# Kernel optimization log

Measured on AMD Instinct MI355X. Metric: run time of the kernel, lower is better.

The kernel has to match this reference:

```python
import jax, jax.numpy as jnp
import numpy as np

B, L, S, C, H = 2, 2048, 2048, 1024, 16
HD = C // H  # head_dim = 64


def setup_inputs() -> dict:
    key = jax.random.key(0)
    k0, k1, k2, k3, k4 = jax.random.split(key, 5)
    w_scale = 1.0 / np.sqrt(C).astype(np.float32)
    return {
        "x0": jax.random.normal(k0, (B, L, C), jnp.float32),
        "x1": jax.random.normal(k1, (B, S, C), jnp.float32),
        "Wqk": jax.random.normal(k2, (C, C), jnp.float32) * w_scale,
        "Wv": jax.random.normal(k3, (C, C), jnp.float32) * w_scale,
        "Wmerge": jax.random.normal(k4, (C, C), jnp.float32) * w_scale,
    }


def reference(x0, x1, Wqk, Wv, Wmerge):
    softmax_temp = HD ** -0.5
    scale = softmax_temp ** 0.5  # applied to both qk0 and qk1

    def split_heads(t):  # [B,N,C] -> [B,N,H,HD]
        return t.reshape(t.shape[0], t.shape[1], H, HD)

    # shared QK projection (same weight for both streams), torch Linear: y = x @ W^T
    qk0 = split_heads(x0 @ Wqk.T) * scale  # [B,L,H,HD]
    qk1 = split_heads(x1 @ Wqk.T) * scale  # [B,S,H,HD]
    v0 = split_heads(x0 @ Wv.T)            # [B,L,H,HD]
    v1 = split_heads(x1 @ Wv.T)            # [B,S,H,HD]

    # single similarity matrix reused for both softmax directions
    sim = jnp.einsum('blhd,bshd->bhls', qk0, qk1)  # [B,H,L,S]
    attn01 = jax.nn.softmax(sim, axis=-1)  # softmax over S (x0 attends x1)
    attn10 = jax.nn.softmax(sim, axis=-2)  # softmax over L (== softmax(sim^T, -1))

    o0 = jnp.einsum('bhls,bshd->blhd', attn01, v1).reshape(x0.shape[0], x0.shape[1], C)
    o1 = jnp.einsum('bhls,blhd->bshd', attn10, v0).reshape(x1.shape[0], x1.shape[1], C)

    return (o0 @ Wmerge.T, o1 @ Wmerge.T)
```

## Files before the change

### kernel.cpp

```cpp
#include <hip/hip_runtime.h>
#include <hip/hip_bf16.h>
#include <stdint.h>


typedef __attribute__((ext_vector_type(8))) short bf16x8;
typedef __attribute__((ext_vector_type(4))) float f32x4;
typedef __attribute__((ext_vector_type(16))) float f32x16;
typedef __attribute__((ext_vector_type(4))) unsigned int u32x4;
typedef __attribute__((ext_vector_type(2))) unsigned int u32x2;
typedef __bf16 bf16_2 __attribute__((ext_vector_type(2)));

typedef const __attribute__((address_space(1))) unsigned int gu32;
typedef __attribute__((address_space(3))) unsigned int lu32;

__device__ __forceinline__ unsigned short f2bf(float f) {
  unsigned int u = __builtin_bit_cast(unsigned int, f);
  u += 0x7fffu + ((u >> 16) & 1u);
  return (unsigned short)(u >> 16);
}

__device__ __forceinline__ unsigned int cvtpk(float lo, float hi_) {
  bf16_2 t = { (__bf16)lo, (__bf16)hi_ };
  return __builtin_bit_cast(unsigned int, t);
}

__device__ __forceinline__ unsigned short f2bf_hw(float f) {
  return __builtin_bit_cast(unsigned short, (__bf16)f);
}

__global__ void cvt_x(const float* __restrict__ x0, const float* __restrict__ x1,
                      unsigned short* __restrict__ dst) {
  const long NX = 4194304;
  int y = blockIdx.y;
  const float* src = y ? x1 : x0;
  long i = ((long)blockIdx.x * 256 + threadIdx.x) * 8;
  float4 a = *(const float4*)(src + i);
  float4 b = *(const float4*)(src + i + 4);
  union { unsigned short u[8]; bf16x8 v; } r;
  r.u[0] = f2bf(a.x); r.u[1] = f2bf(a.y); r.u[2] = f2bf(a.z); r.u[3] = f2bf(a.w);
  r.u[4] = f2bf(b.x); r.u[5] = f2bf(b.y); r.u[6] = f2bf(b.z); r.u[7] = f2bf(b.w);
  *(bf16x8*)(dst + y * NX + i) = r.v;
}

__global__ void cvt_w(const float* __restrict__ w0, const float* __restrict__ w1,
                      const float* __restrict__ w2, unsigned short* __restrict__ dst) {
  const long NW = 1048576;
  int y = blockIdx.y;
  const float* src = (y == 0) ? w0 : ((y == 1) ? w1 : w2);
  long i = ((long)blockIdx.x * 256 + threadIdx.x) * 8;
  float4 a = *(const float4*)(src + i);
  float4 b = *(const float4*)(src + i + 4);
  union { unsigned short u[8]; bf16x8 v; } r;
  r.u[0] = f2bf(a.x); r.u[1] = f2bf(a.y); r.u[2] = f2bf(a.z); r.u[3] = f2bf(a.w);
  r.u[4] = f2bf(b.x); r.u[5] = f2bf(b.y); r.u[6] = f2bf(b.z); r.u[7] = f2bf(b.w);
  *(bf16x8*)(dst + y * NW + i) = r.v;
}

template<int OUTF32>
__global__ __launch_bounds__(256, 2)
void gemm_bt(const unsigned short* __restrict__ A, const unsigned short* __restrict__ B,
             void* __restrict__ C, int M, int N, int K, float scale) {
  __shared__ unsigned short As[128 * 32];
  __shared__ unsigned short Bs[128 * 32];
  const int tid = threadIdx.x;
  const int lane = tid & 63, w = tid >> 6;
  const int il = lane & 15, g = lane >> 4;
  const int wr = w >> 1, wc = w & 1;
  const int bm = blockIdx.y * 128, bn = blockIdx.x * 128;
  f32x4 acc[4][4];
#pragma unroll
  for (int m = 0; m < 4; ++m)
#pragma unroll
    for (int n = 0; n < 4; ++n) acc[m][n] = (f32x4){0.f, 0.f, 0.f, 0.f};

  const int crow = lane >> 2, ccol = (lane & 3) * 8;
  const int ch0 = w * 2, ch1 = w * 2 + 1;
  const unsigned short* pa0 = A + (long)(bm + ch0 * 16 + crow) * K + ccol;
  const unsigned short* pa1 = A + (long)(bm + ch1 * 16 + crow) * K + ccol;
  const unsigned short* pb0 = B + (long)(bn + ch0 * 16 + crow) * K + ccol;
  const unsigned short* pb1 = B + (long)(bn + ch1 * 16 + crow) * K + ccol;

  for (int k0 = 0; k0 < K; k0 += 32) {
    __builtin_amdgcn_global_load_lds((gu32*)(pa0 + k0), (lu32*)(As + ch0 * 512), 16, 0, 0);
    __builtin_amdgcn_global_load_lds((gu32*)(pa1 + k0), (lu32*)(As + ch1 * 512), 16, 0, 0);
    __builtin_amdgcn_global_load_lds((gu32*)(pb0 + k0), (lu32*)(Bs + ch0 * 512), 16, 0, 0);
    __builtin_amdgcn_global_load_lds((gu32*)(pb1 + k0), (lu32*)(Bs + ch1 * 512), 16, 0, 0);
    __syncthreads();
    bf16x8 av[4], bv[4];
#pragma unroll
    for (int m = 0; m < 4; ++m)
      av[m] = *(const bf16x8*)(As + (wr * 64 + m * 16 + il) * 32 + g * 8);
#pragma unroll
    for (int n = 0; n < 4; ++n)
      bv[n] = *(const bf16x8*)(Bs + (wc * 64 + n * 16 + il) * 32 + g * 8);
#pragma unroll
    for (int m = 0; m < 4; ++m)
#pragma unroll
      for (int n = 0; n < 4; ++n)
        acc[m][n] = __builtin_amdgcn_mfma_f32_16x16x32_bf16(av[m], bv[n], acc[m][n], 0, 0, 0);
    __syncthreads();
  }

#pragma unroll
  for (int m = 0; m < 4; ++m) {
    long row0 = bm + wr * 64 + m * 16 + g * 4;
#pragma unroll
    for (int n = 0; n < 4; ++n) {
      long col = bn + wc * 64 + n * 16 + il;
#pragma unroll
      for (int r = 0; r < 4; ++r) {
        float v = acc[m][n][r] * scale;
        if (OUTF32) ((float*)C)[(row0 + r) * (long)N + col] = v;
        else        ((unsigned short*)C)[(row0 + r) * (long)N + col] = f2bf(v);
      }
    }
  }
}


#define QSTAGEA(BUF, MH, TT)                                                              \
  {                                                                                       \
    long kc = (long)(TT) * 64 + sslot * 8;                                                \
    const unsigned short* s0 = Ag + (long)(bm + (MH) * 64 + srow) * 1024 + kc;            \
    const unsigned short* s1 = Ag + (long)(bm + 128 + (MH) * 64 + srow) * 1024 + kc;      \
    __builtin_amdgcn_global_load_lds((gu32*)s0, (lu32*)(smem + ((BUF)*2+(MH))*8192 + dbase), 16, 0, 0);        \
    __builtin_amdgcn_global_load_lds((gu32*)s1, (lu32*)(smem + ((BUF)*2+(MH))*8192 + 4096 + dbase), 16, 0, 0); \
  }

#define QSTAGEB(BUF, NH, TT)                                                              \
  {                                                                                       \
    long kc = (long)(TT) * 64 + sslot * 8;                                                \
    const unsigned short* s0 = Bg + (long)(bnn + ((srow >> 5) * 64) + (NH) * 32 + (srow & 31)) * 1024 + kc;        \
    const unsigned short* s1 = Bg + (long)(bnn + (((64 + srow) >> 5) * 64) + (NH) * 32 + (srow & 31)) * 1024 + kc; \
    __builtin_amdgcn_global_load_lds((gu32*)s0, (lu32*)(smem + 32768 + ((BUF)*2+(NH))*8192 + dbase), 16, 0, 0);        \
    __builtin_amdgcn_global_load_lds((gu32*)s1, (lu32*)(smem + 32768 + ((BUF)*2+(NH))*8192 + 4096 + dbase), 16, 0, 0); \
  }

#define QCOMPUTE(RBUF, MH, NH)                                                            \
  {                                                                                       \
    const unsigned short* Ar = smem + ((RBUF)*2+(MH))*8192 + (wr * 64 + il) * 64;         \
    const unsigned short* Br = smem + 32768 + ((RBUF)*2+(NH))*8192 + (wc * 32 + il) * 64; \
    bf16x8 av[4][2], bv[2][2];                                                            \
    _Pragma("unroll")                                                                     \
    for (int mp = 0; mp < 4; ++mp)                                                        \
      _Pragma("unroll")                                                                   \
      for (int ks = 0; ks < 2; ++ks)                                                      \
        av[mp][ks] = *(const bf16x8*)(Ar + mp * 1024 + (((ks * 4 + g) ^ sw) * 8));        \
    _Pragma("unroll")                                                                     \
    for (int np = 0; np < 2; ++np)                                                        \
      _Pragma("unroll")                                                                   \
      for (int ks = 0; ks < 2; ++ks)                                                      \
        bv[np][ks] = *(const bf16x8*)(Br + np * 1024 + (((ks * 4 + g) ^ sw) * 8));        \
    _Pragma("unroll")                                                                     \
    for (int mp = 0; mp < 4; ++mp)                                                        \
      _Pragma("unroll")                                                                   \
      for (int np = 0; np < 2; ++np) {                                                    \
        acc[(MH)*4+mp][(NH)*2+np] = __builtin_amdgcn_mfma_f32_16x16x32_bf16(av[mp][0], bv[np][0], acc[(MH)*4+mp][(NH)*2+np], 0, 0, 0); \
        acc[(MH)*4+mp][(NH)*2+np] = __builtin_amdgcn_mfma_f32_16x16x32_bf16(av[mp][1], bv[np][1], acc[(MH)*4+mp][(NH)*2+np], 0, 0, 0); \
      }                                                                                   \
  }

#define QEND(W4)                                                                          \
  {                                                                                       \
    if (W4) asm volatile("s_waitcnt vmcnt(4)" ::: "memory");                              \
    asm volatile("" ::: "memory");                                                        \
    __builtin_amdgcn_s_barrier();                                                         \
    asm volatile("" ::: "memory");                                                        \
  }

__global__ __launch_bounds__(512, 2)
void gemm_qkv8(const unsigned short* __restrict__ Ag, const unsigned short* __restrict__ Bg,
               unsigned short* __restrict__ C0, unsigned short* __restrict__ vt, float scale0) {
  extern __shared__ unsigned short smem[];
  const int tid = threadIdx.x;
  const int lane = tid & 63, wid = tid >> 6;
  const int il = lane & 15, g = lane >> 4;
  const int wr = wid >> 2, wc = wid & 3;
  const int sw = il & 7;
  const int bm = blockIdx.y * 256, bnn = blockIdx.x * 256;

  const int srow = tid >> 3;
  const int sslot = (tid & 7) ^ ((tid >> 3) & 7);
  const int dbase = (tid >> 6) * 512;

  f32x4 acc[8][4];
#pragma unroll
  for (int m = 0; m < 8; ++m)
#pragma unroll
    for (int n = 0; n < 4; ++n) acc[m][n] = (f32x4){0.f, 0.f, 0.f, 0.f};

  QSTAGEA(0, 0, 0); QSTAGEA(0, 1, 0); QSTAGEB(0, 0, 0); QSTAGEB(0, 1, 0);
  QSTAGEB(1, 0, 1); QSTAGEA(1, 1, 1);
  __syncthreads();

#pragma unroll 1
  for (int i = 0; i < 8; ++i) {
    const int t1 = 2 * i + 1, t2 = (2 * i + 2) & 15, t3 = (2 * i + 3) & 15;
    QSTAGEA(1, 0, t1); QCOMPUTE(0, 0, 0); QEND(0);
    QSTAGEB(1, 1, t1); QCOMPUTE(0, 1, 0); QEND(0);
    QSTAGEB(0, 0, t2); QCOMPUTE(0, 1, 1); QEND(0);
    QSTAGEA(0, 1, t2); QCOMPUTE(0, 0, 1); QEND(1);
    QSTAGEA(0, 0, t2); QCOMPUTE(1, 0, 0); QEND(0);
    QSTAGEB(0, 1, t2); QCOMPUTE(1, 1, 0); QEND(0);
    QSTAGEB(1, 0, t3); QCOMPUTE(1, 1, 1); QEND(0);
    QSTAGEA(1, 1, t3); QCOMPUTE(1, 0, 1); QEND(1);
  }
  __syncthreads();

  if (bnn < 1024) {
#pragma unroll
    for (int m = 0; m < 8; ++m) {
      long row0 = bm + wr * 128 + m * 16 + g * 4;
#pragma unroll
      for (int n = 0; n < 4; ++n) {
        long col = bnn + wc * 64 + n * 16 + il;
#pragma unroll
        for (int r = 0; r < 4; ++r)
          C0[(row0 + r) * 1024 + col] = f2bf(acc[m][n][r] * scale0);
      }
    }
  } else {
    unsigned short (*T)[264] = (unsigned short (*)[264])smem;
    const int s = bm >> 11;
#pragma unroll 1
    for (int p = 0; p < 2; ++p) {
      if ((wc >> 1) == p) {
#pragma unroll
        for (int m = 0; m < 8; ++m) {
          int rl = wr * 128 + m * 16 + g * 4;
#pragma unroll
          for (int n = 0; n < 4; ++n) {
            int cl = (wc & 1) * 64 + n * 16 + il;
            u32x2 pk = { cvtpk(acc[m][n][0], acc[m][n][1]), cvtpk(acc[m][n][2], acc[m][n][3]) };
            *(u32x2*)&T[cl][rl] = pk;
          }
        }
      }
      __syncthreads();
      int cl2 = tid & 127, portion = tid >> 7;
      int col = (bnn - 1024) + p * 128 + cl2;
      unsigned short* dst = vt + (((long)(s * 16 + (col >> 6))) * 64 + (col & 63)) * 2048
                               + (bm & 2047) + portion * 64;
#pragma unroll
      for (int j = 0; j < 8; ++j)
        *(bf16x8*)(dst + j * 8) = *(const bf16x8*)&T[cl2][portion * 64 + j * 8];
      __syncthreads();
    }
  }
}

__global__ __launch_bounds__(256, 4)
void attn_kernel(const unsigned short* __restrict__ qk,
                 const unsigned short* __restrict__ vt,
                 unsigned short* __restrict__ o) {
  __shared__ unsigned short sK[2][4096];
  __shared__ unsigned short sV[2][4096];
  int bid = blockIdx.x;
  int lb = (bid & 7) * 128 + (bid >> 3);
  int tid = threadIdx.x;
  int w = tid >> 6, lane = tid & 63;
  int u = lb * 4 + w;
  int dir = u >> 11, bh = (u >> 6) & 31, qu = u & 63;
  int b = bh >> 4, h = bh & 15;
  int q = lane & 31, hi = lane >> 5;

  long qrow0 = (dir ? 4096L : 0L) + b * 2048L + (long)qu * 32L;
  long krow0 = (dir ? 0L : 4096L) + b * 2048L;
  int vs = dir ? b : 2 + b;
  long vrow0 = (long)(vs * 16 + h) * 64;

  const unsigned short* Qp = qk + (qrow0 + q) * 1024 + h * 64 + hi * 8;

  int srow = tid >> 3;
  int sc = ((tid & 7) * 8) ^ ((srow & 7) << 3);
  const unsigned short* kg = qk + (krow0 + srow) * 1024 + h * 64 + sc;
  const unsigned short* vg = vt + (vrow0 + srow) * 2048 + sc;
  const int wbase = w * 512;

#define STAGE(BUF, T)                                                                    \
  {                                                                                      \
    long jj = (long)(T) * 64;                                                            \
    __builtin_amdgcn_global_load_lds((gu32*)(kg + jj * 1024),        (lu32*)(sK[BUF] + wbase),        16, 0, 0); \
    __builtin_amdgcn_global_load_lds((gu32*)(kg + (jj + 32) * 1024), (lu32*)(sK[BUF] + wbase + 2048), 16, 0, 0); \
    __builtin_amdgcn_global_load_lds((gu32*)(vg + jj),               (lu32*)(sV[BUF] + wbase),        16, 0, 0); \
    __builtin_amdgcn_global_load_lds((gu32*)(vg + jj + 32 * 2048),   (lu32*)(sV[BUF] + wbase + 2048), 16, 0, 0); \
  }

  bf16x8 qf[4];
#pragma unroll
  for (int ds = 0; ds < 4; ++ds)
    qf[ds] = *(const bf16x8*)(Qp + ds * 16);

  f32x16 z16;
#pragma unroll
  for (int j = 0; j < 16; ++j) z16[j] = 0.f;
  f32x16 accO[2];
  accO[0] = z16; accO[1] = z16;
  f32x16 lsum = z16;
  const short oneb = (short)0x3F80;
  const bf16x8 ones = {oneb, oneb, oneb, oneb, oneb, oneb, oneb, oneb};

  STAGE(0, 0);
  __syncthreads();

#pragma unroll 1
  for (int t = 0; t < 32; ++t) {
    int cur = t & 1;
    if (t < 31) STAGE(cur ^ 1, t + 1);

    bf16x8 kf[8], vf[8];
    int cswz = (q & 7) << 3;
#pragma unroll
    for (int kb = 0; kb < 2; ++kb)
#pragma unroll
      for (int ds = 0; ds < 4; ++ds)
        kf[kb * 4 + ds] = *(const bf16x8*)(&sK[cur][(kb * 32 + q) * 64 + ((ds * 16 + hi * 8) ^ cswz)]);
#pragma unroll
    for (int ks = 0; ks < 4; ++ks)
#pragma unroll
      for (int dn = 0; dn < 2; ++dn)
        vf[ks * 2 + dn] = *(const bf16x8*)(&sV[cur][(dn * 32 + q) * 64 + ((ks * 16 + hi * 8) ^ cswz)]);

    f32x16 st0 = __builtin_amdgcn_mfma_f32_32x32x16_bf16(kf[0], qf[0], z16, 0, 0, 0);
    f32x16 st1 = __builtin_amdgcn_mfma_f32_32x32x16_bf16(kf[4], qf[0], z16, 0, 0, 0);
#pragma unroll
    for (int ds = 1; ds < 4; ++ds)
      st0 = __builtin_amdgcn_mfma_f32_32x32x16_bf16(kf[ds], qf[ds], st0, 0, 0, 0);
#pragma unroll
    for (int ds = 1; ds < 4; ++ds)
      st1 = __builtin_amdgcn_mfma_f32_32x32x16_bf16(kf[4 + ds], qf[ds], st1, 0, 0, 0);

#pragma unroll
    for (int j = 0; j < 16; ++j) {
      st0[j] = __builtin_amdgcn_exp2f(st0[j]);
      st1[j] = __builtin_amdgcn_exp2f(st1[j]);
    }

    bf16x8 pa[4];
#pragma unroll
    for (int ks = 0; ks < 4; ++ks) {
      int m0 = (ks & 1) * 8;
      unsigned int a0, a1, b0, b1;
      if (ks < 2) {
        a0 = cvtpk(st0[m0],     st0[m0 + 1]); a1 = cvtpk(st0[m0 + 2], st0[m0 + 3]);
        b0 = cvtpk(st0[m0 + 4], st0[m0 + 5]); b1 = cvtpk(st0[m0 + 6], st0[m0 + 7]);
      } else {
        a0 = cvtpk(st1[m0],     st1[m0 + 1]); a1 = cvtpk(st1[m0 + 2], st1[m0 + 3]);
        b0 = cvtpk(st1[m0 + 4], st1[m0 + 5]); b1 = cvtpk(st1[m0 + 6], st1[m0 + 7]);
      }
      u32x2 r0 = __builtin_amdgcn_permlane32_swap(a0, b0, false, false);
      u32x2 r1 = __builtin_amdgcn_permlane32_swap(a1, b1, false, false);
      u32x4 uu = {r0[0], r1[0], r0[1], r1[1]};
      pa[ks] = __builtin_bit_cast(bf16x8, uu);
    }
#pragma unroll
    for (int ks = 0; ks < 4; ++ks)
      lsum = __builtin_amdgcn_mfma_f32_32x32x16_bf16(pa[ks], ones, lsum, 0, 0, 0);
#pragma unroll
    for (int ks = 0; ks < 4; ++ks)
#pragma unroll
      for (int dn = 0; dn < 2; ++dn)
        accO[dn] = __builtin_amdgcn_mfma_f32_32x32x16_bf16(pa[ks], vf[ks * 2 + dn], accO[dn], 0, 0, 0);

    __syncthreads();
  }
#undef STAGE

#pragma unroll
  for (int r = 0; r < 16; ++r) {
    int row = (r & 3) + 8 * (r >> 2) + 4 * hi;
    float invr = 1.f / lsum[r];
    long orow = qrow0 + row;
#pragma unroll
    for (int dn = 0; dn < 2; ++dn)
      o[orow * 1024 + h * 64 + dn * 32 + q] = f2bf_hw(accO[dn][r] * invr);
  }
}

extern "C" void kernel_launch(void* const* d_in, const int* in_sizes, int n_in,
                              void* d_out, int out_size, void* d_ws, size_t ws_size,
                              hipStream_t stream) {
  const float* x0 = (const float*)d_in[0];
  const float* x1 = (const float*)d_in[1];
  const float* Wqk = (const float*)d_in[2];
  const float* Wv = (const float*)d_in[3];
  const float* Wm = (const float*)d_in[4];
  float* out = (float*)d_out;

  const long NX = 4194304;
  const long NW = 1048576;
  unsigned short* xb  = (unsigned short*)d_ws;
  unsigned short* wb  = xb + 2 * NX;
  unsigned short* qkb = wb + 3 * NW;
  unsigned short* vb  = qkb + 2 * NX;
  unsigned short* vtb = vb + 2 * NX;

  cvt_x<<<dim3(2048, 2), 256, 0, stream>>>(x0, x1, xb);
  cvt_w<<<dim3(512, 3), 256, 0, stream>>>(Wqk, Wv, Wm, wb);

  const float sqk = 0.35355339059327373f * 1.2011224087864498f;
  gemm_qkv8<<<dim3(8, 32), 512, 131072, stream>>>(xb, wb, qkb, vtb, sqk);
  attn_kernel<<<1024, 256, 0, stream>>>(qkb, vtb, vb);
  gemm_bt<1><<<dim3(8, 64), 256, 0, stream>>>(vb, wb + 2 * NW, out, 8192, 1024, 1024, 1.f);
}
```

Measured before the change: 161.8 us.

## Replace merge projection GEMM with pipelined 256x128 swizzled async-load kernel

Drops the simple single-buffered 128x128 gemm_bt used for the output merge projection. In its place is a 512-thread gemm_merge8 that reuses the QKV GEMM's multi-stage async global-to-LDS pipeline, with XOR-swizzled LDS, a 256x128 tile and a 64-wide K step. The QEND macro now takes a parameterized vmcnt so the new kernel can wait for its different number of outstanding loads. The aim is to hide global load latency and cut barrier stalls in the final GEMM, at the cost of more LDS per block and lower occupancy.

```diff
diff --git a/kernel.cpp b/kernel.cpp
--- a/kernel.cpp
+++ b/kernel.cpp
@@ -56,67 +56,6 @@
   *(bf16x8*)(dst + y * NW + i) = r.v;
 }
 
-template<int OUTF32>
-__global__ __launch_bounds__(256, 2)
-void gemm_bt(const unsigned short* __restrict__ A, const unsigned short* __restrict__ B,
-             void* __restrict__ C, int M, int N, int K, float scale) {
-  __shared__ unsigned short As[128 * 32];
-  __shared__ unsigned short Bs[128 * 32];
-  const int tid = threadIdx.x;
-  const int lane = tid & 63, w = tid >> 6;
-  const int il = lane & 15, g = lane >> 4;
-  const int wr = w >> 1, wc = w & 1;
-  const int bm = blockIdx.y * 128, bn = blockIdx.x * 128;
-  f32x4 acc[4][4];
-#pragma unroll
-  for (int m = 0; m < 4; ++m)
-#pragma unroll
-    for (int n = 0; n < 4; ++n) acc[m][n] = (f32x4){0.f, 0.f, 0.f, 0.f};
-
-  const int crow = lane >> 2, ccol = (lane & 3) * 8;
-  const int ch0 = w * 2, ch1 = w * 2 + 1;
-  const unsigned short* pa0 = A + (long)(bm + ch0 * 16 + crow) * K + ccol;
-  const unsigned short* pa1 = A + (long)(bm + ch1 * 16 + crow) * K + ccol;
-  const unsigned short* pb0 = B + (long)(bn + ch0 * 16 + crow) * K + ccol;
-  const unsigned short* pb1 = B + (long)(bn + ch1 * 16 + crow) * K + ccol;
-
-  for (int k0 = 0; k0 < K; k0 += 32) {
-    __builtin_amdgcn_global_load_lds((gu32*)(pa0 + k0), (lu32*)(As + ch0 * 512), 16, 0, 0);
-    __builtin_amdgcn_global_load_lds((gu32*)(pa1 + k0), (lu32*)(As + ch1 * 512), 16, 0, 0);
-    __builtin_amdgcn_global_load_lds((gu32*)(pb0 + k0), (lu32*)(Bs + ch0 * 512), 16, 0, 0);
-    __builtin_amdgcn_global_load_lds((gu32*)(pb1 + k0), (lu32*)(Bs + ch1 * 512), 16, 0, 0);
-    __syncthreads();
-    bf16x8 av[4], bv[4];
-#pragma unroll
-    for (int m = 0; m < 4; ++m)
-      av[m] = *(const bf16x8*)(As + (wr * 64 + m * 16 + il) * 32 + g * 8);
-#pragma unroll
-    for (int n = 0; n < 4; ++n)
-      bv[n] = *(const bf16x8*)(Bs + (wc * 64 + n * 16 + il) * 32 + g * 8);
-#pragma unroll
-    for (int m = 0; m < 4; ++m)
-#pragma unroll
-      for (int n = 0; n < 4; ++n)
-        acc[m][n] = __builtin_amdgcn_mfma_f32_16x16x32_bf16(av[m], bv[n], acc[m][n], 0, 0, 0);
-    __syncthreads();
-  }
-
-#pragma unroll
-  for (int m = 0; m < 4; ++m) {
-    long row0 = bm + wr * 64 + m * 16 + g * 4;
-#pragma unroll
-    for (int n = 0; n < 4; ++n) {
-      long col = bn + wc * 64 + n * 16 + il;
-#pragma unroll
-      for (int r = 0; r < 4; ++r) {
-        float v = acc[m][n][r] * scale;
-        if (OUTF32) ((float*)C)[(row0 + r) * (long)N + col] = v;
-        else        ((unsigned short*)C)[(row0 + r) * (long)N + col] = f2bf(v);
-      }
-    }
-  }
-}
-
 
 #define QSTAGEA(BUF, MH, TT)                                                              \
   {                                                                                       \
@@ -160,9 +99,9 @@
       }                                                                                   \
   }
 
-#define QEND(W4)                                                                          \
-  {                                                                                       \
-    if (W4) asm volatile("s_waitcnt vmcnt(4)" ::: "memory");                              \
+#define QEND(W4, N4)                                                                      \
+  {                                                                                       \
+    if (W4) asm volatile("s_waitcnt vmcnt(" #N4 ")" ::: "memory");                        \
     asm volatile("" ::: "memory");                                                        \
     __builtin_amdgcn_s_barrier();                                                         \
     asm volatile("" ::: "memory");                                                        \
@@ -196,14 +135,14 @@
 #pragma unroll 1
   for (int i = 0; i < 8; ++i) {
     const int t1 = 2 * i + 1, t2 = (2 * i + 2) & 15, t3 = (2 * i + 3) & 15;
-    QSTAGEA(1, 0, t1); QCOMPUTE(0, 0, 0); QEND(0);
-    QSTAGEB(1, 1, t1); QCOMPUTE(0, 1, 0); QEND(0);
-    QSTAGEB(0, 0, t2); QCOMPUTE(0, 1, 1); QEND(0);
-    QSTAGEA(0, 1, t2); QCOMPUTE(0, 0, 1); QEND(1);
-    QSTAGEA(0, 0, t2); QCOMPUTE(1, 0, 0); QEND(0);
-    QSTAGEB(0, 1, t2); QCOMPUTE(1, 1, 0); QEND(0);
-    QSTAGEB(1, 0, t3); QCOMPUTE(1, 1, 1); QEND(0);
-    QSTAGEA(1, 1, t3); QCOMPUTE(1, 0, 1); QEND(1);
+    QSTAGEA(1, 0, t1); QCOMPUTE(0, 0, 0); QEND(0, 0);
+    QSTAGEB(1, 1, t1); QCOMPUTE(0, 1, 0); QEND(0, 0);
+    QSTAGEB(0, 0, t2); QCOMPUTE(0, 1, 1); QEND(0, 0);
+    QSTAGEA(0, 1, t2); QCOMPUTE(0, 0, 1); QEND(1, 4);
+    QSTAGEA(0, 0, t2); QCOMPUTE(1, 0, 0); QEND(0, 0);
+    QSTAGEB(0, 1, t2); QCOMPUTE(1, 1, 0); QEND(0, 0);
+    QSTAGEB(1, 0, t3); QCOMPUTE(1, 1, 1); QEND(0, 0);
+    QSTAGEA(1, 1, t3); QCOMPUTE(1, 0, 1); QEND(1, 4);
   }
   __syncthreads();
 
@@ -245,6 +184,87 @@
       for (int j = 0; j < 8; ++j)
         *(bf16x8*)(dst + j * 8) = *(const bf16x8*)&T[cl2][portion * 64 + j * 8];
       __syncthreads();
+    }
+  }
+}
+
+
+#define MSTAGEB(BUF, NH, TT)                                                              \
+  {                                                                                       \
+    long kc = (long)(TT) * 64 + sslot * 8;                                                \
+    const unsigned short* s0 = Bg + (long)(bnn + ((srow >> 4) * 32) + (NH) * 16 + (srow & 15)) * 1024 + kc; \
+    __builtin_amdgcn_global_load_lds((gu32*)s0, (lu32*)(smem + 32768 + ((BUF)*2+(NH))*4096 + dbase2), 16, 0, 0); \
+  }
+
+#define MCOMPUTE(RBUF, MH, NH)                                                            \
+  {                                                                                       \
+    const unsigned short* Ar = smem + ((RBUF)*2+(MH))*8192 + (wr * 64 + il) * 64;         \
+    const unsigned short* Br = smem + 32768 + ((RBUF)*2+(NH))*4096 + (wc * 16 + il) * 64; \
+    bf16x8 av[4][2], bv[2];                                                               \
+    _Pragma("unroll")                                                                     \
+    for (int mp = 0; mp < 4; ++mp)                                                        \
+      _Pragma("unroll")                                                                   \
+      for (int ks = 0; ks < 2; ++ks)                                                      \
+        av[mp][ks] = *(const bf16x8*)(Ar + mp * 1024 + (((ks * 4 + g) ^ sw) * 8));        \
+    _Pragma("unroll")                                                                     \
+    for (int ks = 0; ks < 2; ++ks)                                                        \
+      bv[ks] = *(const bf16x8*)(Br + (((ks * 4 + g) ^ sw) * 8));                          \
+    _Pragma("unroll")                                                                     \
+    for (int mp = 0; mp < 4; ++mp) {                                                      \
+      acc[(MH)*4+mp][(NH)] = __builtin_amdgcn_mfma_f32_16x16x32_bf16(av[mp][0], bv[0], acc[(MH)*4+mp][(NH)], 0, 0, 0); \
+      acc[(MH)*4+mp][(NH)] = __builtin_amdgcn_mfma_f32_16x16x32_bf16(av[mp][1], bv[1], acc[(MH)*4+mp][(NH)], 0, 0, 0); \
+    }                                                                                     \
+  }
+
+__global__ __launch_bounds__(512, 2)
+void gemm_merge8(const unsigned short* __restrict__ Ag, const unsigned short* __restrict__ Bg,
+                 float* __restrict__ C) {
+  extern __shared__ unsigned short smem[];
+  const int tid = threadIdx.x;
+  const int lane = tid & 63, wid = tid >> 6;
+  const int il = lane & 15, g = lane >> 4;
+  const int wr = wid >> 2, wc = wid & 3;
+  const int sw = il & 7;
+  const int bm = blockIdx.y * 256, bnn = blockIdx.x * 128;
+
+  const int srow = tid >> 3;
+  const int sslot = (tid & 7) ^ ((tid >> 3) & 7);
+  const int dbase = (tid >> 6) * 512;
+  const int dbase2 = tid * 8;
+
+  f32x4 acc[8][2];
+#pragma unroll
+  for (int m = 0; m < 8; ++m)
+#pragma unroll
+    for (int n = 0; n < 2; ++n) acc[m][n] = (f32x4){0.f, 0.f, 0.f, 0.f};
+
+  QSTAGEA(0, 0, 0); QSTAGEA(0, 1, 0); MSTAGEB(0, 0, 0); MSTAGEB(0, 1, 0);
+  MSTAGEB(1, 0, 1); QSTAGEA(1, 1, 1);
+  __syncthreads();
+
+#pragma unroll 1
+  for (int i = 0; i < 8; ++i) {
+    const int t1 = 2 * i + 1, t2 = (2 * i + 2) & 15, t3 = (2 * i + 3) & 15;
+    QSTAGEA(1, 0, t1); MCOMPUTE(0, 0, 0); QEND(0, 0);
+    MSTAGEB(1, 1, t1); MCOMPUTE(0, 1, 0); QEND(0, 0);
+    MSTAGEB(0, 0, t2); MCOMPUTE(0, 1, 1); QEND(0, 0);
+    QSTAGEA(0, 1, t2); MCOMPUTE(0, 0, 1); QEND(1, 3);
+    QSTAGEA(0, 0, t2); MCOMPUTE(1, 0, 0); QEND(0, 0);
+    MSTAGEB(0, 1, t2); MCOMPUTE(1, 1, 0); QEND(0, 0);
+    MSTAGEB(1, 0, t3); MCOMPUTE(1, 1, 1); QEND(0, 0);
+    QSTAGEA(1, 1, t3); MCOMPUTE(1, 0, 1); QEND(1, 3);
+  }
+  __syncthreads();
+
+#pragma unroll
+  for (int m = 0; m < 8; ++m) {
+    long row0 = bm + wr * 128 + m * 16 + g * 4;
+#pragma unroll
+    for (int n = 0; n < 2; ++n) {
+      long col = bnn + wc * 32 + n * 16 + il;
+#pragma unroll
+      for (int r = 0; r < 4; ++r)
+        C[(row0 + r) * 1024 + col] = acc[m][n][r];
     }
   }
 }
@@ -401,5 +421,5 @@
   const float sqk = 0.35355339059327373f * 1.2011224087864498f;
   gemm_qkv8<<<dim3(8, 32), 512, 131072, stream>>>(xb, wb, qkb, vtb, sqk);
   attn_kernel<<<1024, 256, 0, stream>>>(qkb, vtb, vb);
-  gemm_bt<1><<<dim3(8, 64), 256, 0, stream>>>(vb, wb + 2 * NW, out, 8192, 1024, 1024, 1.f);
-}
+  gemm_merge8<<<dim3(8, 32), 512, 98304, stream>>>(vb, wb + 2 * NW, out);
+}
```

Result: no change. 158.9 us (-1.8%).
